# Optimization experiments

Hardware: AMD Instinct MI355X
Metric: run time of the kernel (lower is better)

## Reference

```python
import jax, jax.numpy as jnp
import numpy as np

B, S, D, H = 2, 2048, 1024, 16
HD = D // H
EPS = 1e-5
THETA = 10000.0


def _rope_freqs(seq_len, dim, dtype=jnp.float32):
    inv_freq = 1.0 / (THETA ** (np.arange(0, dim, 2)[: dim // 2] / dim))
    t = np.arange(seq_len)
    freqs = np.outer(t, inv_freq)  # [S, dim//2]
    return jnp.asarray(np.cos(freqs), dtype), jnp.asarray(np.sin(freqs), dtype)


def _apply_rope(x, cos, sin):
    # x: [B, S, H, HD]; cos/sin: [S, HD//2]
    x_even = x[..., 0::2]
    x_odd = x[..., 1::2]
    cos = cos.reshape(1, x.shape[1], 1, -1)
    sin = sin.reshape(1, x.shape[1], 1, -1)
    out_even = x_even * cos - x_odd * sin
    out_odd = x_even * sin + x_odd * cos
    return jnp.stack([out_even, out_odd], axis=-1).reshape(x.shape)


def setup_inputs() -> dict:
    key = jax.random.key(0)
    ks = jax.random.split(key, 6)
    s = 1.0 / np.sqrt(D)
    return {
        "x": jax.random.normal(ks[0], (B, S, D), jnp.float32),
        "Wq": jax.random.normal(ks[1], (D, D), jnp.float32) * s,
        "Wk": jax.random.normal(ks[2], (D, D), jnp.float32) * s,
        "Wv": jax.random.normal(ks[3], (D, D), jnp.float32) * s,
        "Wo": jax.random.normal(ks[4], (D, D), jnp.float32) * s,
        "alpha": jnp.ones((1,), jnp.float32),
    }


def reference(x, Wq, Wk, Wv, Wo, alpha):
    b, s, d = x.shape
    q = (x @ Wq).reshape(b, s, H, HD)
    k = (x @ Wk).reshape(b, s, H, HD)
    v = (x @ Wv).reshape(b, s, H, HD)

    cos, sin = _rope_freqs(s, HD, x.dtype)
    q = _apply_rope(q, cos, sin)
    k = _apply_rope(k, cos, sin)

    # YAT score: (q.k)^2 / (||q-k||^2 + eps)
    qk = jnp.einsum("bqhd,bkhd->bhqk", q, k)            # [B,H,S,S]
    qn = jnp.sum(q * q, axis=-1)                          # [B,S,H]
    kn = jnp.sum(k * k, axis=-1)                          # [B,S,H]
    dist2 = (qn.transpose(0, 2, 1)[:, :, :, None]
             + kn.transpose(0, 2, 1)[:, :, None, :]
             - 2.0 * qk)                                   # [B,H,S,S]
    scores = (qk * qk) / (dist2 + EPS)

    # alpha scaling: (sqrt(head_dim)/log(1+head_dim))^alpha
    scale = (jnp.sqrt(jnp.float32(HD)) / jnp.log(jnp.float32(1 + HD))) ** alpha[0]
    scores = scores * scale

    # causal mask
    causal = jnp.tril(jnp.ones((s, s), bool))
    big_neg = jnp.finfo(scores.dtype).min
    scores = jnp.where(causal[None, None, :, :], scores, big_neg)

    attn = jax.nn.softmax(scores, axis=-1)
    out = jnp.einsum("bhqk,bkhd->bqhd", attn, v).reshape(b, s, d)
    return out @ Wo
```

## Files before the change

### kernel.cpp

```cpp
#include <hip/hip_runtime.h>
#include <cmath>

#define BB 2
#define SS 2048
#define DD 1024
#define HH 16
#define HDD 64
#define MM (BB * SS)
#define BH (BB * HH)

typedef _Float16 f16;
typedef _Float16 f16x2 __attribute__((ext_vector_type(2)));
typedef _Float16 f16x4 __attribute__((ext_vector_type(4)));
typedef _Float16 f16x8 __attribute__((ext_vector_type(8)));
typedef float f32x4 __attribute__((ext_vector_type(4)));
typedef float f32x16 __attribute__((ext_vector_type(16)));
typedef unsigned int u32x4 __attribute__((ext_vector_type(4)));

#define MFMA(A, B, C) __builtin_amdgcn_mfma_f32_16x16x32_f16(A, B, C, 0, 0, 0)
#define MFMA32(A, B, C) __builtin_amdgcn_mfma_f32_32x32x16_f16(A, B, C, 0, 0, 0)

__device__ __forceinline__ void gload16(const void* g, void* l) {
    __builtin_amdgcn_global_load_lds(
        (const __attribute__((address_space(1))) void*)g,
        (__attribute__((address_space(3))) void*)l, 16, 0, 0);
}

__device__ __forceinline__ unsigned pk(float a, float b) {
    auto h = __builtin_amdgcn_cvt_pkrtz(a, b);
    return __builtin_bit_cast(unsigned, h);
}

__device__ __forceinline__ f16x8 pack8(float p0, float p1, float p2, float p3,
                                       float p4, float p5, float p6, float p7,
                                       int hi) {
    unsigned wa = pk(p0, p1), wa2 = pk(p2, p3);
    unsigned wb = pk(p4, p5), wb2 = pk(p6, p7);
    unsigned xa = __shfl_xor(wa, 32), xa2 = __shfl_xor(wa2, 32);
    unsigned xb = __shfl_xor(wb, 32), xb2 = __shfl_xor(wb2, 32);
    unsigned w0 = hi ? xb : wa;
    unsigned w1 = hi ? xb2 : wa2;
    unsigned w2 = hi ? wb : xa;
    unsigned w3 = hi ? wb2 : xa2;
    u32x4 w = {w0, w1, w2, w3};
    return __builtin_bit_cast(f16x8, w);
}

__global__ __launch_bounds__(256) void k_rope_table(float* __restrict__ cosT,
                                                    float* __restrict__ sinT) {
    int idx = blockIdx.x * 256 + threadIdx.x;
    int s = idx >> 5, j = idx & 31;
    double inv = pow(10000.0, -(double)(2 * j) / 64.0);
    double ang = (double)s * inv;
    cosT[idx] = (float)cos(ang);
    sinT[idx] = (float)sin(ang);
}

__global__ __launch_bounds__(256) void k_cast_x(const float* __restrict__ x,
                                                f16* __restrict__ xb) {
    int i = (blockIdx.x * 256 + threadIdx.x) * 8;
    float4 a = *(const float4*)&x[i];
    float4 b = *(const float4*)&x[i + 4];
    f16x8 o = {(f16)a.x, (f16)a.y, (f16)a.z, (f16)a.w,
               (f16)b.x, (f16)b.y, (f16)b.z, (f16)b.w};
    *(f16x8*)&xb[i] = o;
}

__global__ __launch_bounds__(256) void k_wcast(const float* __restrict__ Wq,
        const float* __restrict__ Wk, const float* __restrict__ Wv,
        const float* __restrict__ Wo, f16* __restrict__ WtAll) {
    const int z = blockIdx.z;
    const float* __restrict__ src = (z == 0) ? Wq : (z == 1) ? Wk
                                   : (z == 2) ? Wv : Wo;
    f16* __restrict__ dst = WtAll + (size_t)z * DD * DD;
    const int kk0 = blockIdx.x * 64, nn0 = blockIdx.y * 64;
    __shared__ float t[64][65];
    const int tid = threadIdx.x;
    const int rr = tid >> 4, c4 = (tid & 15) * 4;
#pragma unroll
    for (int p = 0; p < 4; ++p) {
        float4 v = *(const float4*)&src[(size_t)(kk0 + p * 16 + rr) * DD + nn0 + c4];
        t[p * 16 + rr][c4 + 0] = v.x; t[p * 16 + rr][c4 + 1] = v.y;
        t[p * 16 + rr][c4 + 2] = v.z; t[p * 16 + rr][c4 + 3] = v.w;
    }
    __syncthreads();
#pragma unroll
    for (int p = 0; p < 4; ++p) {
        int n = p * 16 + rr;
        f16x4 o = {(f16)t[c4 + 0][n], (f16)t[c4 + 1][n],
                   (f16)t[c4 + 2][n], (f16)t[c4 + 3][n]};
        *(f16x4*)&dst[(size_t)(nn0 + n) * DD + kk0 + c4] = o;
    }
}

__global__ __launch_bounds__(256) void k_qkv(const f16* __restrict__ xb,
        const f16* __restrict__ WtAll,
        const float* __restrict__ cosT, const float* __restrict__ sinT,
        f16* __restrict__ Qh, f16* __restrict__ Kh, f16* __restrict__ Vh,
        float* __restrict__ qn, float* __restrict__ kn) {
    const int z = blockIdx.z;
    const f16* __restrict__ Wt = WtAll + (size_t)z * DD * DD;
    f16* __restrict__ dst = (z == 0) ? Qh : (z == 1) ? Kh : Vh;
    const int m0 = blockIdx.x * 128;
    const int n0 = blockIdx.y * 128;
    __shared__ f16 As[128 * 32];
    __shared__ f16 Bs[128 * 32];
    const int tid = threadIdx.x;
    const int wv = tid >> 6, ln = tid & 63;
    const int wm = wv >> 1, wn = wv & 1;
    const int lg = ln >> 4, lr = ln & 15;
    f32x4 acc[4][4] = {};
    for (int k0 = 0; k0 < DD; k0 += 32) {
        __syncthreads();
#pragma unroll
        for (int u = 0; u < 2; ++u) {
            int e = u * 2048 + wv * 512 + ln * 8;
            int r = e >> 5, c = e & 31;
            gload16(&xb[(size_t)(m0 + r) * DD + k0 + c], &As[e]);
            gload16(&Wt[(size_t)(n0 + r) * DD + k0 + c], &Bs[e]);
        }
        __syncthreads();
        f16x8 af[4], bf[4];
#pragma unroll
        for (int mt = 0; mt < 4; ++mt)
            af[mt] = *(const f16x8*)&As[(wm * 64 + mt * 16 + lr) * 32 + lg * 8];
#pragma unroll
        for (int nt = 0; nt < 4; ++nt)
            bf[nt] = *(const f16x8*)&Bs[(wn * 64 + nt * 16 + lr) * 32 + lg * 8];
#pragma unroll
        for (int mt = 0; mt < 4; ++mt)
#pragma unroll
            for (int nt = 0; nt < 4; ++nt)
                acc[mt][nt] = MFMA(af[mt], bf[nt], acc[mt][nt]);
    }
    const bool isv = (z == 2);
#pragma unroll
    for (int mt = 0; mt < 4; ++mt) {
        float nsum[4] = {0.f, 0.f, 0.f, 0.f};
#pragma unroll
        for (int reg = 0; reg < 4; ++reg) {
            int gr = m0 + wm * 64 + mt * 16 + lg * 4 + reg;
            int b = gr >> 11, s = gr & (SS - 1);
#pragma unroll
            for (int nt = 0; nt < 4; ++nt) {
                int gc = n0 + wn * 64 + nt * 16 + lr;
                int h = gc >> 6, d = gc & 63;
                float v = acc[mt][nt][reg];
                if (!isv) {
                    float p = __shfl_xor(v, 1);
                    int pr = d >> 1;
                    float cz = cosT[s * 32 + pr], sz = sinT[s * 32 + pr];
                    if ((lr & 1) == 0) {
                        float oe = v * cz - p * sz;
                        float oo = v * sz + p * cz;
                        f16x2 st; st[0] = (f16)oe; st[1] = (f16)oo;
                        *(f16x2*)&dst[(((size_t)b * HH + h) * SS + s) * HDD + d] = st;
                        nsum[reg] += oe * oe + oo * oo;
                    }
                } else {
                    dst[(((size_t)b * HH + h) * SS + s) * HDD + d] = (f16)v;
                }
            }
        }
        if (!isv) {
#pragma unroll
            for (int reg = 0; reg < 4; ++reg) {
                float ns = nsum[reg];
                ns += __shfl_xor(ns, 1); ns += __shfl_xor(ns, 2);
                ns += __shfl_xor(ns, 4); ns += __shfl_xor(ns, 8);
                if (lr == 0) {
                    int gr = m0 + wm * 64 + mt * 16 + lg * 4 + reg;
                    int b = gr >> 11, s = gr & (SS - 1);
                    int h = (n0 + wn * 64) >> 6;
                    float* np = (z == 0) ? qn : kn;
                    np[((size_t)b * HH + h) * SS + s] = ns;
                }
            }
        }
    }
}

__global__ __launch_bounds__(256) void k_vt(const f16* __restrict__ Vh,
                                            f16* __restrict__ Vt) {
    const int s0 = blockIdx.x * 64;
    const int bh = blockIdx.y;
    __shared__ f16 t[64][80];
    const int tid = threadIdx.x;
    const int sr = tid >> 3, d0 = (tid & 7) * 8;
#pragma unroll
    for (int p = 0; p < 2; ++p) {
        f16x8 v = *(const f16x8*)&Vh[((size_t)bh * SS + s0 + p * 32 + sr) * HDD + d0];
#pragma unroll
        for (int j = 0; j < 8; ++j) t[d0 + j][p * 32 + sr] = v[j];
    }
    __syncthreads();
    const int dr = tid >> 3, s4 = (tid & 7) * 8;
#pragma unroll
    for (int p = 0; p < 2; ++p) {
        f16x8 o = *(const f16x8*)&t[p * 32 + dr][s4];
        *(f16x8*)&Vt[((size_t)bh * HDD + p * 32 + dr) * SS + s0 + s4] = o;
    }
}

__global__ __launch_bounds__(256, 2) void k_attn(const f16* __restrict__ Qh,
        const f16* __restrict__ Kh, const f16* __restrict__ Vt,
        const float* __restrict__ qn, const float* __restrict__ kn,
        const float* __restrict__ alpha, f16* __restrict__ AO) {
    const int tid = threadIdx.x;
    const int wv = tid >> 6, ln = tid & 63;
    const int task = blockIdx.x * 4 + wv;
    const int bh = task & (BH - 1);
    const int qb = (SS / 32 - 1) - (task >> 5);
    const int lq = ln & 31, hi = ln >> 5;
    const int q0 = qb * 32;
    const float scl = powf(8.0f / logf(65.0f), alpha[0]);
    const f16* __restrict__ Qp = Qh + (size_t)bh * SS * HDD;
    const f16* __restrict__ Kp = Kh + (size_t)bh * SS * HDD;
    const f16* __restrict__ Vp = Vt + (size_t)bh * HDD * SS;
    const float* __restrict__ knp = kn + (size_t)bh * SS;

    f16x8 qf[4];
#pragma unroll
    for (int dt = 0; dt < 4; ++dt)
        qf[dt] = *(const f16x8*)&Qp[(size_t)(q0 + lq) * HDD + dt * 16 + hi * 8];
    const float qnl = qn[(size_t)bh * SS + q0 + lq] + 1e-5f;

    float m_ = -INFINITY, l_ = 0.f;
    f32x16 o0 = {}, o1 = {};
    const int ktd = qb >> 1;
    const int qg = q0 + lq;

    auto body = [&](int kb, bool tri0, bool tri1, bool use1) {
        f32x16 s0 = {}, s1 = {};
#pragma unroll
        for (int dt = 0; dt < 4; ++dt) {
            f16x8 kf = *(const f16x8*)&Kp[(size_t)(kb + lq) * HDD + dt * 16 + hi * 8];
            s0 = MFMA32(kf, qf[dt], s0);
        }
        if (use1) {
#pragma unroll
            for (int dt = 0; dt < 4; ++dt) {
                f16x8 kf = *(const f16x8*)&Kp[(size_t)(kb + 32 + lq) * HDD + dt * 16 + hi * 8];
                s1 = MFMA32(kf, qf[dt], s1);
            }
        }
        float4 kn0[4], kn1[4];
#pragma unroll
        for (int g = 0; g < 4; ++g)
            kn0[g] = *(const float4*)&knp[kb + 8 * g + 4 * hi];
        if (use1) {
#pragma unroll
            for (int g = 0; g < 4; ++g)
                kn1[g] = *(const float4*)&knp[kb + 32 + 8 * g + 4 * hi];
        }
#pragma unroll
        for (int r = 0; r < 16; ++r) {
            const int koff = (r & 3) + 8 * (r >> 2) + 4 * hi;
            float qk = s0[r];
            float d2 = qnl + kn0[r >> 2][r & 3] - 2.f * qk;
            float sc = qk * qk * scl * __builtin_amdgcn_rcpf(d2);
            if (tri0 && (kb + koff > qg)) sc = -3.0e38f;
            s0[r] = sc;
            if (use1) {
                float qk1 = s1[r];
                float d21 = qnl + kn1[r >> 2][r & 3] - 2.f * qk1;
                float sc1 = qk1 * qk1 * scl * __builtin_amdgcn_rcpf(d21);
                if (tri1 && (kb + 32 + koff > qg)) sc1 = -3.0e38f;
                s1[r] = sc1;
            }
        }
        float mx = -3.0e38f;
#pragma unroll
        for (int r = 0; r < 16; ++r) mx = fmaxf(mx, s0[r]);
        if (use1) {
#pragma unroll
            for (int r = 0; r < 16; ++r) mx = fmaxf(mx, s1[r]);
        }
        mx = fmaxf(mx, __shfl_xor(mx, 32));
        if (__any(mx > m_)) {
            float mnew = fmaxf(m_, mx);
            float corr = __expf(m_ - mnew);
            m_ = mnew;
            l_ *= corr;
#pragma unroll
            for (int r = 0; r < 16; ++r) {
                float cr = __shfl(corr, (r & 3) + 8 * (r >> 2) + 4 * hi);
                o0[r] *= cr; o1[r] *= cr;
            }
        }
        float ps = 0.f;
#pragma unroll
        for (int r = 0; r < 16; ++r) {
            float p = __expf(s0[r] - m_); s0[r] = p; ps += p;
        }
        if (use1) {
#pragma unroll
            for (int r = 0; r < 16; ++r) {
                float p = __expf(s1[r] - m_); s1[r] = p; ps += p;
            }
        }
        ps += __shfl_xor(ps, 32);
        l_ += ps;
        f16x8 pa0 = pack8(s0[0], s0[1], s0[2], s0[3], s0[4], s0[5], s0[6], s0[7], hi);
        f16x8 pa1 = pack8(s0[8], s0[9], s0[10], s0[11], s0[12], s0[13], s0[14], s0[15], hi);
#pragma unroll
        for (int k16 = 0; k16 < 2; ++k16) {
            f16x8 pa = k16 ? pa1 : pa0;
            f16x8 vf0 = *(const f16x8*)&Vp[(size_t)lq * SS + kb + k16 * 16 + hi * 8];
            f16x8 vf1 = *(const f16x8*)&Vp[(size_t)(32 + lq) * SS + kb + k16 * 16 + hi * 8];
            o0 = MFMA32(pa, vf0, o0);
            o1 = MFMA32(pa, vf1, o1);
        }
        if (use1) {
            f16x8 pb0 = pack8(s1[0], s1[1], s1[2], s1[3], s1[4], s1[5], s1[6], s1[7], hi);
            f16x8 pb1 = pack8(s1[8], s1[9], s1[10], s1[11], s1[12], s1[13], s1[14], s1[15], hi);
#pragma unroll
            for (int k16 = 0; k16 < 2; ++k16) {
                f16x8 pb = k16 ? pb1 : pb0;
                f16x8 vf0 = *(const f16x8*)&Vp[(size_t)lq * SS + kb + 32 + k16 * 16 + hi * 8];
                f16x8 vf1 = *(const f16x8*)&Vp[(size_t)(32 + lq) * SS + kb + 32 + k16 * 16 + hi * 8];
                o0 = MFMA32(pb, vf0, o0);
                o1 = MFMA32(pb, vf1, o1);
            }
        }
    };

    for (int kt = 0; kt < ktd; ++kt) body(kt * 64, false, false, true);
    {
        const bool odd = (qb & 1) != 0;
        body(ktd * 64, !odd, odd, odd);
    }

    float li = 1.0f / l_;
#pragma unroll
    for (int r = 0; r < 16; ++r) {
        int qlo = (r & 3) + 8 * (r >> 2) + 4 * hi;
        float lir = __shfl(li, qlo);
        size_t row = (size_t)bh * SS + q0 + qlo;
        AO[row * HDD + lq] = (f16)(o0[r] * lir);
        AO[row * HDD + 32 + lq] = (f16)(o1[r] * lir);
    }
}

__global__ __launch_bounds__(256) void k_proj(const f16* __restrict__ AO,
        const f16* __restrict__ Wot, float* __restrict__ out) {
    const int m0 = blockIdx.x * 128;
    const int n0 = blockIdx.y * 128;
    __shared__ f16 As[128 * 32];
    __shared__ f16 Bs[128 * 32];
    const int tid = threadIdx.x;
    const int wv = tid >> 6, ln = tid & 63;
    const int wm = wv >> 1, wn = wv & 1;
    const int lg = ln >> 4, lr = ln & 15;
    f32x4 acc[4][4] = {};
    for (int k0 = 0; k0 < DD; k0 += 32) {
        __syncthreads();
#pragma unroll
        for (int u = 0; u < 2; ++u) {
            int e = u * 2048 + wv * 512 + ln * 8;
            int r = e >> 5, c = e & 31;
            int gm = m0 + r, b = gm >> 11, s = gm & (SS - 1);
            int k = k0 + c, h = k >> 6, d = k & 63;
            gload16(&AO[(((size_t)b * HH + h) * SS + s) * HDD + d], &As[e]);
            gload16(&Wot[(size_t)(n0 + r) * DD + k0 + c], &Bs[e]);
        }
        __syncthreads();
        f16x8 af[4], bf[4];
#pragma unroll
        for (int mt = 0; mt < 4; ++mt)
            af[mt] = *(const f16x8*)&As[(wm * 64 + mt * 16 + lr) * 32 + lg * 8];
#pragma unroll
        for (int nt = 0; nt < 4; ++nt)
            bf[nt] = *(const f16x8*)&Bs[(wn * 64 + nt * 16 + lr) * 32 + lg * 8];
#pragma unroll
        for (int mt = 0; mt < 4; ++mt)
#pragma unroll
            for (int nt = 0; nt < 4; ++nt)
                acc[mt][nt] = MFMA(af[mt], bf[nt], acc[mt][nt]);
    }
#pragma unroll
    for (int mt = 0; mt < 4; ++mt)
#pragma unroll
        for (int reg = 0; reg < 4; ++reg) {
            int gr = m0 + wm * 64 + mt * 16 + lg * 4 + reg;
#pragma unroll
            for (int nt = 0; nt < 4; ++nt) {
                int gc = n0 + wn * 64 + nt * 16 + lr;
                out[(size_t)gr * DD + gc] = acc[mt][nt][reg];
            }
        }
}

extern "C" void kernel_launch(void* const* d_in, const int* in_sizes, int n_in,
                              void* d_out, int out_size, void* d_ws, size_t ws_size,
                              hipStream_t stream) {
    const float* x     = (const float*)d_in[0];
    const float* Wq    = (const float*)d_in[1];
    const float* Wk    = (const float*)d_in[2];
    const float* Wv    = (const float*)d_in[3];
    const float* Wo    = (const float*)d_in[4];
    const float* alpha = (const float*)d_in[5];
    float* out = (float*)d_out;

    float* cosT = (float*)d_ws;
    float* sinT = cosT + SS * 32;
    float* qn   = sinT + SS * 32;
    float* kn   = qn + (size_t)BH * SS;
    f16* xb     = (f16*)(kn + (size_t)BH * SS);
    f16* WtAll  = xb + (size_t)MM * DD;
    f16* Qh     = WtAll + (size_t)4 * DD * DD;
    f16* Kh     = Qh + (size_t)MM * DD;
    f16* Vh     = Kh + (size_t)MM * DD;
    f16* Vt     = Vh + (size_t)MM * DD;
    f16* AO     = Vt + (size_t)MM * DD;
    f16* Wot    = WtAll + (size_t)3 * DD * DD;

    hipLaunchKernelGGL(k_rope_table, dim3(SS * 32 / 256), dim3(256), 0, stream,
                       cosT, sinT);
    hipLaunchKernelGGL(k_cast_x, dim3(MM * DD / (256 * 8)), dim3(256), 0, stream,
                       x, xb);
    hipLaunchKernelGGL(k_wcast, dim3(16, 16, 4), dim3(256), 0, stream,
                       Wq, Wk, Wv, Wo, WtAll);
    hipLaunchKernelGGL(k_qkv, dim3(MM / 128, DD / 128, 3), dim3(256), 0, stream,
                       xb, WtAll, cosT, sinT, Qh, Kh, Vh, qn, kn);
    hipLaunchKernelGGL(k_vt, dim3(SS / 64, BH), dim3(256), 0, stream, Vh, Vt);
    hipLaunchKernelGGL(k_attn, dim3((SS / 32) * BH / 4), dim3(256), 0, stream,
                       Qh, Kh, Vt, qn, kn, alpha, AO);
    hipLaunchKernelGGL(k_proj, dim3(MM / 128, DD / 128), dim3(256), 0, stream,
                       AO, Wot, out);
}
```

Baseline: 290.6 us.

## Split attention KV loop across four waves per query block with LDS merge

Each query block of 32 rows is now handled by a whole 4-wave workgroup. The waves interleave the 32-key tiles and their partial softmax states are merged through shared memory, instead of one wave walking the whole causal range alone. The intent is to shorten the serial per-wave dependency chain and balance work. K tiles are also prefetched one iteration ahead, and rescaling is skipped until the running max grows by more than 8. In addition, q norms are computed in-kernel from the fp16 Q fragments and k norms are stored as fp16, which costs some precision and adds LDS traffic and a barrier.

```diff
diff --git a/kernel.cpp b/kernel.cpp
--- a/kernel.cpp
+++ b/kernel.cpp
@@ -97,7 +97,7 @@
         const f16* __restrict__ WtAll,
         const float* __restrict__ cosT, const float* __restrict__ sinT,
         f16* __restrict__ Qh, f16* __restrict__ Kh, f16* __restrict__ Vh,
-        float* __restrict__ qn, float* __restrict__ kn) {
+        f16* __restrict__ knh) {
     const int z = blockIdx.z;
     const f16* __restrict__ Wt = WtAll + (size_t)z * DD * DD;
     f16* __restrict__ dst = (z == 0) ? Qh : (z == 1) ? Kh : Vh;
@@ -155,14 +155,14 @@
                         float oo = v * sz + p * cz;
                         f16x2 st; st[0] = (f16)oe; st[1] = (f16)oo;
                         *(f16x2*)&dst[(((size_t)b * HH + h) * SS + s) * HDD + d] = st;
-                        nsum[reg] += oe * oe + oo * oo;
+                        if (z == 1) nsum[reg] += oe * oe + oo * oo;
                     }
                 } else {
                     dst[(((size_t)b * HH + h) * SS + s) * HDD + d] = (f16)v;
                 }
             }
         }
-        if (!isv) {
+        if (z == 1) {
 #pragma unroll
             for (int reg = 0; reg < 4; ++reg) {
                 float ns = nsum[reg];
@@ -172,8 +172,7 @@
                     int gr = m0 + wm * 64 + mt * 16 + lg * 4 + reg;
                     int b = gr >> 11, s = gr & (SS - 1);
                     int h = (n0 + wn * 64) >> 6;
-                    float* np = (z == 0) ? qn : kn;
-                    np[((size_t)b * HH + h) * SS + s] = ns;
+                    knh[((size_t)b * HH + h) * SS + s] = (f16)ns;
                 }
             }
         }
@@ -202,86 +201,87 @@
     }
 }
 
-__global__ __launch_bounds__(256, 2) void k_attn(const f16* __restrict__ Qh,
+__global__ __launch_bounds__(256, 4) void k_attn(const f16* __restrict__ Qh,
         const f16* __restrict__ Kh, const f16* __restrict__ Vt,
-        const float* __restrict__ qn, const float* __restrict__ kn,
+        const f16* __restrict__ knh,
         const float* __restrict__ alpha, f16* __restrict__ AO) {
     const int tid = threadIdx.x;
     const int wv = tid >> 6, ln = tid & 63;
-    const int task = blockIdx.x * 4 + wv;
-    const int bh = task & (BH - 1);
-    const int qb = (SS / 32 - 1) - (task >> 5);
     const int lq = ln & 31, hi = ln >> 5;
+    const int blk = blockIdx.x;
+    const int bh = blk & (BH - 1);
+    const int qb = (SS / 32 - 1) - (blk >> 5);
     const int q0 = qb * 32;
     const float scl = powf(8.0f / logf(65.0f), alpha[0]);
     const f16* __restrict__ Qp = Qh + (size_t)bh * SS * HDD;
     const f16* __restrict__ Kp = Kh + (size_t)bh * SS * HDD;
     const f16* __restrict__ Vp = Vt + (size_t)bh * HDD * SS;
-    const float* __restrict__ knp = kn + (size_t)bh * SS;
+    const f16* __restrict__ knp = knh + (size_t)bh * SS;
+
+    __shared__ float oL[4][32][68];
+    __shared__ float mlL[4][2][32];
 
     f16x8 qf[4];
 #pragma unroll
     for (int dt = 0; dt < 4; ++dt)
         qf[dt] = *(const f16x8*)&Qp[(size_t)(q0 + lq) * HDD + dt * 16 + hi * 8];
-    const float qnl = qn[(size_t)bh * SS + q0 + lq] + 1e-5f;
+    float qn = 0.f;
+#pragma unroll
+    for (int dt = 0; dt < 4; ++dt)
+#pragma unroll
+        for (int j = 0; j < 8; ++j) {
+            float v = (float)qf[dt][j];
+            qn = fmaf(v, v, qn);
+        }
+    qn += __shfl_xor(qn, 32);
+    const float qnl = qn + 1e-5f;
 
     float m_ = -INFINITY, l_ = 0.f;
     f32x16 o0 = {}, o1 = {};
-    const int ktd = qb >> 1;
-    const int qg = q0 + lq;
-
-    auto body = [&](int kb, bool tri0, bool tri1, bool use1) {
-        f32x16 s0 = {}, s1 = {};
-#pragma unroll
-        for (int dt = 0; dt < 4; ++dt) {
-            f16x8 kf = *(const f16x8*)&Kp[(size_t)(kb + lq) * HDD + dt * 16 + hi * 8];
-            s0 = MFMA32(kf, qf[dt], s0);
-        }
-        if (use1) {
-#pragma unroll
-            for (int dt = 0; dt < 4; ++dt) {
-                f16x8 kf = *(const f16x8*)&Kp[(size_t)(kb + 32 + lq) * HDD + dt * 16 + hi * 8];
-                s1 = MFMA32(kf, qf[dt], s1);
-            }
-        }
-        float4 kn0[4], kn1[4];
+    f16x8 kf[4];
+
+    if (wv < qb) {
+        int kb = wv * 32;
+#pragma unroll
+        for (int dt = 0; dt < 4; ++dt)
+            kf[dt] = *(const f16x8*)&Kp[(size_t)(kb + lq) * HDD + dt * 16 + hi * 8];
+    }
+
+    auto tile = [&](int kb, bool diag, bool pre, int kbn) {
+        f16x8 vf0 = *(const f16x8*)&Vp[(size_t)lq * SS + kb + hi * 8];
+        f16x8 vf1 = *(const f16x8*)&Vp[(size_t)lq * SS + kb + 16 + hi * 8];
+        f16x8 vf2 = *(const f16x8*)&Vp[(size_t)(32 + lq) * SS + kb + hi * 8];
+        f16x8 vf3 = *(const f16x8*)&Vp[(size_t)(32 + lq) * SS + kb + 16 + hi * 8];
+        f16x4 knv[4];
 #pragma unroll
         for (int g = 0; g < 4; ++g)
-            kn0[g] = *(const float4*)&knp[kb + 8 * g + 4 * hi];
-        if (use1) {
-#pragma unroll
-            for (int g = 0; g < 4; ++g)
-                kn1[g] = *(const float4*)&knp[kb + 32 + 8 * g + 4 * hi];
+            knv[g] = *(const f16x4*)&knp[kb + 8 * g + 4 * hi];
+        f32x16 s = {};
+#pragma unroll
+        for (int dt = 0; dt < 4; ++dt) s = MFMA32(kf[dt], qf[dt], s);
+        if (pre) {
+#pragma unroll
+            for (int dt = 0; dt < 4; ++dt)
+                kf[dt] = *(const f16x8*)&Kp[(size_t)(kbn + lq) * HDD + dt * 16 + hi * 8];
         }
 #pragma unroll
         for (int r = 0; r < 16; ++r) {
             const int koff = (r & 3) + 8 * (r >> 2) + 4 * hi;
-            float qk = s0[r];
-            float d2 = qnl + kn0[r >> 2][r & 3] - 2.f * qk;
+            float qk = s[r];
+            float kv = (float)knv[r >> 2][r & 3];
+            float d2 = qnl + kv - 2.0f * qk;
             float sc = qk * qk * scl * __builtin_amdgcn_rcpf(d2);
-            if (tri0 && (kb + koff > qg)) sc = -3.0e38f;
-            s0[r] = sc;
-            if (use1) {
-                float qk1 = s1[r];
-                float d21 = qnl + kn1[r >> 2][r & 3] - 2.f * qk1;
-                float sc1 = qk1 * qk1 * scl * __builtin_amdgcn_rcpf(d21);
-                if (tri1 && (kb + 32 + koff > qg)) sc1 = -3.0e38f;
-                s1[r] = sc1;
-            }
+            if (diag && koff > lq) sc = -3.0e38f;
+            s[r] = sc;
         }
         float mx = -3.0e38f;
 #pragma unroll
-        for (int r = 0; r < 16; ++r) mx = fmaxf(mx, s0[r]);
-        if (use1) {
-#pragma unroll
-            for (int r = 0; r < 16; ++r) mx = fmaxf(mx, s1[r]);
-        }
+        for (int r = 0; r < 16; ++r) mx = fmaxf(mx, s[r]);
         mx = fmaxf(mx, __shfl_xor(mx, 32));
-        if (__any(mx > m_)) {
+        if (__any(mx > m_ + 8.0f)) {
             float mnew = fmaxf(m_, mx);
             float corr = __expf(m_ - mnew);
-            m_ = mnew;
-            l_ *= corr;
+            m_ = mnew; l_ *= corr;
 #pragma unroll
             for (int r = 0; r < 16; ++r) {
                 float cr = __shfl(corr, (r & 3) + 8 * (r >> 2) + 4 * hi);
@@ -291,54 +291,69 @@
         float ps = 0.f;
 #pragma unroll
         for (int r = 0; r < 16; ++r) {
-            float p = __expf(s0[r] - m_); s0[r] = p; ps += p;
-        }
-        if (use1) {
-#pragma unroll
-            for (int r = 0; r < 16; ++r) {
-                float p = __expf(s1[r] - m_); s1[r] = p; ps += p;
-            }
+            float p = __expf(s[r] - m_); s[r] = p; ps += p;
         }
         ps += __shfl_xor(ps, 32);
         l_ += ps;
-        f16x8 pa0 = pack8(s0[0], s0[1], s0[2], s0[3], s0[4], s0[5], s0[6], s0[7], hi);
-        f16x8 pa1 = pack8(s0[8], s0[9], s0[10], s0[11], s0[12], s0[13], s0[14], s0[15], hi);
-#pragma unroll
-        for (int k16 = 0; k16 < 2; ++k16) {
-            f16x8 pa = k16 ? pa1 : pa0;
-            f16x8 vf0 = *(const f16x8*)&Vp[(size_t)lq * SS + kb + k16 * 16 + hi * 8];
-            f16x8 vf1 = *(const f16x8*)&Vp[(size_t)(32 + lq) * SS + kb + k16 * 16 + hi * 8];
-            o0 = MFMA32(pa, vf0, o0);
-            o1 = MFMA32(pa, vf1, o1);
-        }
-        if (use1) {
-            f16x8 pb0 = pack8(s1[0], s1[1], s1[2], s1[3], s1[4], s1[5], s1[6], s1[7], hi);
-            f16x8 pb1 = pack8(s1[8], s1[9], s1[10], s1[11], s1[12], s1[13], s1[14], s1[15], hi);
-#pragma unroll
-            for (int k16 = 0; k16 < 2; ++k16) {
-                f16x8 pb = k16 ? pb1 : pb0;
-                f16x8 vf0 = *(const f16x8*)&Vp[(size_t)lq * SS + kb + 32 + k16 * 16 + hi * 8];
-                f16x8 vf1 = *(const f16x8*)&Vp[(size_t)(32 + lq) * SS + kb + 32 + k16 * 16 + hi * 8];
-                o0 = MFMA32(pb, vf0, o0);
-                o1 = MFMA32(pb, vf1, o1);
-            }
-        }
+        f16x8 pa0 = pack8(s[0], s[1], s[2], s[3], s[4], s[5], s[6], s[7], hi);
+        f16x8 pa1 = pack8(s[8], s[9], s[10], s[11], s[12], s[13], s[14], s[15], hi);
+        o0 = MFMA32(pa0, vf0, o0);
+        o0 = MFMA32(pa1, vf1, o0);
+        o1 = MFMA32(pa0, vf2, o1);
+        o1 = MFMA32(pa1, vf3, o1);
     };
 
-    for (int kt = 0; kt < ktd; ++kt) body(kt * 64, false, false, true);
+    for (int kt = wv; kt < qb; kt += 4) {
+        const bool pre = (kt + 4 < qb);
+        tile(kt * 32, false, pre, pre ? (kt + 4) * 32 : 0);
+    }
+    if ((qb & 3) == wv) {
+        int kb = qb * 32;
+#pragma unroll
+        for (int dt = 0; dt < 4; ++dt)
+            kf[dt] = *(const f16x8*)&Kp[(size_t)(kb + lq) * HDD + dt * 16 + hi * 8];
+        tile(kb, true, false, 0);
+    }
+
+#pragma unroll
+    for (int r = 0; r < 16; ++r) {
+        int q = (r & 3) + 8 * (r >> 2) + 4 * hi;
+        oL[wv][q][lq] = o0[r];
+        oL[wv][q][32 + lq] = o1[r];
+    }
+    if (hi == 0) { mlL[wv][0][lq] = m_; mlL[wv][1][lq] = l_; }
+    __syncthreads();
     {
-        const bool odd = (qb & 1) != 0;
-        body(ktd * 64, !odd, odd, odd);
-    }
-
-    float li = 1.0f / l_;
-#pragma unroll
-    for (int r = 0; r < 16; ++r) {
-        int qlo = (r & 3) + 8 * (r >> 2) + 4 * hi;
-        float lir = __shfl(li, qlo);
-        size_t row = (size_t)bh * SS + q0 + qlo;
-        AO[row * HDD + lq] = (f16)(o0[r] * lir);
-        AO[row * HDD + 32 + lq] = (f16)(o1[r] * lir);
+        const int q = tid >> 3, d8 = (tid & 7) * 8;
+        float mv[4], lv[4];
+#pragma unroll
+        for (int i = 0; i < 4; ++i) { mv[i] = mlL[i][0][q]; lv[i] = mlL[i][1][q]; }
+        float M = fmaxf(fmaxf(mv[0], mv[1]), fmaxf(mv[2], mv[3]));
+        float fac[4], L = 0.f;
+#pragma unroll
+        for (int i = 0; i < 4; ++i) {
+            fac[i] = __expf(mv[i] - M);
+            L = fmaf(lv[i], fac[i], L);
+        }
+        float rL = 1.0f / L;
+        float acc[8] = {};
+#pragma unroll
+        for (int i = 0; i < 4; ++i) {
+            float4 a = *(const float4*)&oL[i][q][d8];
+            float4 b = *(const float4*)&oL[i][q][d8 + 4];
+            acc[0] = fmaf(a.x, fac[i], acc[0]);
+            acc[1] = fmaf(a.y, fac[i], acc[1]);
+            acc[2] = fmaf(a.z, fac[i], acc[2]);
+            acc[3] = fmaf(a.w, fac[i], acc[3]);
+            acc[4] = fmaf(b.x, fac[i], acc[4]);
+            acc[5] = fmaf(b.y, fac[i], acc[5]);
+            acc[6] = fmaf(b.z, fac[i], acc[6]);
+            acc[7] = fmaf(b.w, fac[i], acc[7]);
+        }
+        f16x8 st;
+#pragma unroll
+        for (int j = 0; j < 8; ++j) st[j] = (f16)(acc[j] * rL);
+        *(f16x8*)&AO[((size_t)bh * SS + q0 + q) * HDD + d8] = st;
     }
 }
 
@@ -404,9 +419,8 @@
 
     float* cosT = (float*)d_ws;
     float* sinT = cosT + SS * 32;
-    float* qn   = sinT + SS * 32;
-    float* kn   = qn + (size_t)BH * SS;
-    f16* xb     = (f16*)(kn + (size_t)BH * SS);
+    f16* knh    = (f16*)(sinT + SS * 32);
+    f16* xb     = knh + (size_t)BH * SS;
     f16* WtAll  = xb + (size_t)MM * DD;
     f16* Qh     = WtAll + (size_t)4 * DD * DD;
     f16* Kh     = Qh + (size_t)MM * DD;
@@ -422,10 +436,10 @@
     hipLaunchKernelGGL(k_wcast, dim3(16, 16, 4), dim3(256), 0, stream,
                        Wq, Wk, Wv, Wo, WtAll);
     hipLaunchKernelGGL(k_qkv, dim3(MM / 128, DD / 128, 3), dim3(256), 0, stream,
-                       xb, WtAll, cosT, sinT, Qh, Kh, Vh, qn, kn);
+                       xb, WtAll, cosT, sinT, Qh, Kh, Vh, knh);
     hipLaunchKernelGGL(k_vt, dim3(SS / 64, BH), dim3(256), 0, stream, Vh, Vt);
-    hipLaunchKernelGGL(k_attn, dim3((SS / 32) * BH / 4), dim3(256), 0, stream,
-                       Qh, Kh, Vt, qn, kn, alpha, AO);
+    hipLaunchKernelGGL(k_attn, dim3((SS / 32) * BH), dim3(256), 0, stream,
+                       Qh, Kh, Vt, knh, alpha, AO);
     hipLaunchKernelGGL(k_proj, dim3(MM / 128, DD / 128), dim3(256), 0, stream,
                        AO, Wot, out);
 }
```

Result: faster. 259.4 us (-10.8%).
